# Kernel optimization log

Measured on AMD Instinct MI355X. Metric: run time of the kernel, lower is better.

## Reference

```python
import jax, jax.numpy as jnp
import numpy as np

B, T, E = 8, 2048, 1024
H = 16
HD = E // H            # per-head hidden_dim = 64
DFF = 4 * E
DC = T // 512          # decay_constant = 4
EPS = 1e-5


def setup_inputs() -> dict:
    key = jax.random.key(0)
    ks = jax.random.split(key, 8)
    return {
        "x": jax.random.normal(ks[0], (B, T, E), jnp.float32),
        # per-head input projections (Linear(dim, hidden_dim) x H)
        "w_proj": jax.random.normal(ks[1], (H, E, HD), jnp.float32) / np.sqrt(E),
        "b_proj": jnp.zeros((H, HD), jnp.float32),
        # causal mixing weights: first H//2 heads are Col-repeat, last H//2 Row-repeat
        "mix_w": jax.random.normal(ks[2], (H, T), jnp.float32),
        "mix_b": jnp.zeros((H, T), jnp.float32),
        "decay": jnp.ones((H,), jnp.float32),   # decay_value params (init ones as in torch)
        "out_w": jax.random.normal(ks[3], (E, E), jnp.float32) / np.sqrt(E),
        "out_b": jnp.zeros((E,), jnp.float32),
        "ln1_g": jnp.ones((E,), jnp.float32),
        "ln1_b": jnp.zeros((E,), jnp.float32),
        "ln2_g": jnp.ones((E,), jnp.float32),
        "ln2_b": jnp.zeros((E,), jnp.float32),
        "ff_w1": jax.random.normal(ks[4], (E, DFF), jnp.float32) / np.sqrt(E),
        "ff_b1": jnp.zeros((DFF,), jnp.float32),
        "ff_w2": jax.random.normal(ks[5], (DFF, E), jnp.float32) / np.sqrt(DFF),
        "ff_b2": jnp.zeros((E,), jnp.float32),
        "index": 0,
    }


def _layernorm(x, g, b):
    mu = jnp.mean(x, -1, keepdims=True)
    var = jnp.var(x, -1, keepdims=True)
    return (x - mu) * jax.lax.rsqrt(var + EPS) * g + b


def _mix_matrices(mix_w, decay):
    # Col heads: M[i,j] = v[j] * d**((j-i)/DC) for j>=i else 0
    # Row heads: M[i,j] = v[i] * d**((j-i)/DC) for j>=i else 0
    i = jnp.arange(T)[:, None]
    j = jnp.arange(T)[None, :]
    d = jnp.clip(decay, 0.9, 1.0)                                   # (H,)
    expo = (j - i).astype(jnp.float32) / DC                         # (T,T)
    dec = d[:, None, None] ** expo                                  # (H,T,T)
    causal = (j >= i)
    half = H // 2
    Mcol = jnp.where(causal, mix_w[:half, None, :] * dec[:half], 0.0)
    Mrow = jnp.where(causal, mix_w[half:, :, None] * dec[half:], 0.0)
    return jnp.concatenate([Mcol, Mrow], axis=0)                    # (H,T,T)


def reference(x, w_proj, b_proj, mix_w, mix_b, decay, out_w, out_b,
              ln1_g, ln1_b, ln2_g, ln2_b, ff_w1, ff_b1, ff_w2, ff_b2, index):
    # ---- token-mixing sub-block (parallel path of MixedRepeatHeads) ----
    res = x
    h = _layernorm(x, ln1_g, ln1_b)
    # per-head projection: (B,T,E) x (H,E,HD) -> (B,H,T,HD)
    p = jnp.einsum('bte,hef->bhtf', h, w_proj) + b_proj[:, None, :]
    M = _mix_matrices(mix_w, decay)
    # causal decay mixing along time: out[b,h,s,f] = sum_t p[b,h,t,f] * M[h,t,s]
    mixed = jnp.einsum('bhtf,hts->bhsf', p, M) + mix_b[None, :, :, None]
    # concat heads along feature dim -> (B,T,E)
    mixed = mixed.transpose(0, 2, 1, 3).reshape(B, T, E)
    mixed = mixed @ out_w + out_b
    x = mixed + res
    # ---- feed-forward sub-block ----
    res = x
    h = _layernorm(x, ln2_g, ln2_b)
    h = jax.nn.gelu(h @ ff_w1 + ff_b1) @ ff_w2 + ff_b2
    return h + res
```

## Files before the change

kernel.cpp:

```cpp
#include <hip/hip_runtime.h>


#define TT 2048
#define EE 1024
#define HHD 64
#define MROWS 16384
#define SC_L 64

typedef __bf16 bf16x8 __attribute__((ext_vector_type(8)));
typedef float f32x4 __attribute__((ext_vector_type(4)));
typedef unsigned short u16;
typedef unsigned int u32;

__device__ __forceinline__ u16 f2bf(float f) {
  u32 u = __builtin_bit_cast(u32, f);
  u += 0x7FFFu + ((u >> 16) & 1u);
  return (u16)(u >> 16);
}
__device__ __forceinline__ float bf2f(u16 s) {
  u32 u = ((u32)s) << 16;
  return __builtin_bit_cast(float, u);
}
__device__ __forceinline__ float gelu_f(float x) {
  float x2 = x * x;
  float e = -1.5957691216057308f * x * __builtin_fmaf(0.044715f, x2, 1.0f);
  return x * __builtin_amdgcn_rcpf(1.0f + __expf(e));
}
__device__ __forceinline__ void gload_lds16(const void* g, void* l) {
  __builtin_amdgcn_global_load_lds(
      (const __attribute__((address_space(1))) u32*)g,
      (__attribute__((address_space(3))) u32*)l, 16, 0, 0);
}
__device__ __forceinline__ void wg_barrier() {
  asm volatile("" ::: "memory");
  __builtin_amdgcn_s_barrier();
  asm volatile("" ::: "memory");
}

__global__ __launch_bounds__(256) void transpose_to_bf16(
    const float* __restrict__ src, u16* __restrict__ dst, int R, int C,
    long sbs, long dbs) {
  __shared__ float tile[32][33];
  src += (long)blockIdx.z * sbs;
  dst += (long)blockIdx.z * dbs;
  int c0 = blockIdx.x * 32, r0 = blockIdx.y * 32;
  int tx = threadIdx.x, ty = threadIdx.y;
#pragma unroll
  for (int i = 0; i < 4; i++)
    tile[ty + i * 8][tx] = src[(long)(r0 + ty + i * 8) * C + c0 + tx];
  __syncthreads();
#pragma unroll
  for (int i = 0; i < 4; i++)
    dst[(long)(c0 + ty + i * 8) * R + r0 + tx] = f2bf(tile[tx][ty + i * 8]);
}

__global__ __launch_bounds__(256) void ln_to_bf16(
    const float* __restrict__ x, const float* __restrict__ gam,
    const float* __restrict__ bet, u16* __restrict__ y) {
  int row = blockIdx.x;
  int tid = threadIdx.x;
  float4 v = ((const float4*)x)[row * 256 + tid];
  float s = v.x + v.y + v.z + v.w;
  float s2 = v.x * v.x + v.y * v.y + v.z * v.z + v.w * v.w;
#pragma unroll
  for (int off = 1; off < 64; off <<= 1) {
    s += __shfl_xor(s, off);
    s2 += __shfl_xor(s2, off);
  }
  __shared__ float red[8];
  int w = tid >> 6;
  if ((tid & 63) == 0) { red[w] = s; red[4 + w] = s2; }
  __syncthreads();
  s = red[0] + red[1] + red[2] + red[3];
  s2 = red[4] + red[5] + red[6] + red[7];
  float mu = s * (1.0f / 1024.0f);
  float var = s2 * (1.0f / 1024.0f) - mu * mu;
  float rstd = rsqrtf(var + 1e-5f);
  int e0 = tid * 4;
  ushort4 o;
  o.x = f2bf((v.x - mu) * rstd * gam[e0 + 0] + bet[e0 + 0]);
  o.y = f2bf((v.y - mu) * rstd * gam[e0 + 1] + bet[e0 + 1]);
  o.z = f2bf((v.z - mu) * rstd * gam[e0 + 2] + bet[e0 + 2]);
  o.w = f2bf((v.w - mu) * rstd * gam[e0 + 3] + bet[e0 + 3]);
  ((ushort4*)y)[row * 256 + tid] = o;
}

template <int EPI>
__global__ __launch_bounds__(512, 2) void gemm256(
    const u16* __restrict__ A, const u16* __restrict__ Bt,
    const float* __restrict__ bias, const float* __restrict__ res, void* outp,
    int M, int N, int K, int px, int gxp, int byper) {
  __shared__ u16 lds[65536];
  const int tid = threadIdx.x;
  const int w = tid >> 6, lane = tid & 63;
  const int wm = w >> 2, wn = w & 3;
  const int l15 = lane & 15, lk = lane >> 4;

  const int gx = (int)gridDim.x;
  const int bid = (int)blockIdx.y * gx + (int)blockIdx.x;
  const int xcd = bid & 7, i = bid >> 3;
  const int xg = xcd % gxp, yg = xcd / gxp;
  const int bx = xg * px + (i % px);
  const int by = yg * byper + (i / px);
  const int m0 = by * 256, n0 = bx * 256;

  const int srow = w * 8 + (lane >> 3);
  const int sslot = (lane & 7) ^ (lane >> 3);
  const u16* aS = A + (size_t)(m0 + srow) * K + sslot * 8;
  const u16* bS = Bt + (size_t)(n0 + srow) * K + sslot * 8;

  f32x4 acc[8][4];
  const f32x4 z = {0.f, 0.f, 0.f, 0.f};
#pragma unroll
  for (int mi = 0; mi < 8; mi++)
#pragma unroll
    for (int ni = 0; ni < 4; ni++) acc[mi][ni] = z;

  const int sl0 = (lk ^ (l15 & 7)) * 8;
  const int sl1 = ((4 + lk) ^ (l15 & 7)) * 8;

#define STAGE_ALL(C, KT) { \
    u16* lb = lds + (C) * 32768 + w * 512; \
    gload_lds16(bS + (KT), lb + 16384); \
    gload_lds16(bS + (size_t)64 * K + (KT), lb + 20480); \
    gload_lds16(bS + (size_t)128 * K + (KT), lb + 24576); \
    gload_lds16(bS + (size_t)192 * K + (KT), lb + 28672); \
    gload_lds16(aS + (KT), lb); \
    gload_lds16(aS + (size_t)64 * K + (KT), lb + 4096); \
    gload_lds16(aS + (size_t)128 * K + (KT), lb + 8192); \
    gload_lds16(aS + (size_t)192 * K + (KT), lb + 12288); }

  const int nt = K >> 6;
  STAGE_ALL(0, 0);

  for (int t = 0; t < nt; ++t) {
    const int cur = t & 1, nx = cur ^ 1;
    if (t + 1 < nt) {
      STAGE_ALL(nx, (t + 1) << 6);
      asm volatile("s_waitcnt vmcnt(8)" ::: "memory");
    } else {
      asm volatile("s_waitcnt vmcnt(0)" ::: "memory");
    }
    wg_barrier();

    const u16* lA = lds + cur * 32768;
    const u16* lB = lA + 16384;
    bf16x8 bq0[4], bq1[4];
    {
      const u16* bp = lB + (wn * 64 + l15) * 64;
#pragma unroll
      for (int ni = 0; ni < 4; ni++) {
        bq0[ni] = *(const bf16x8*)(bp + ni * 1024 + sl0);
        bq1[ni] = *(const bf16x8*)(bp + ni * 1024 + sl1);
      }
    }
#pragma unroll
    for (int mi = 0; mi < 8; mi++) {
      const u16* ap = lA + (wm * 128 + mi * 16 + l15) * 64;
      bf16x8 a0 = *(const bf16x8*)(ap + sl0);
      bf16x8 a1 = *(const bf16x8*)(ap + sl1);
      __builtin_amdgcn_s_setprio(1);
#pragma unroll
      for (int ni = 0; ni < 4; ni++)
        acc[mi][ni] = __builtin_amdgcn_mfma_f32_16x16x32_bf16(a0, bq0[ni],
                                                              acc[mi][ni], 0, 0, 0);
#pragma unroll
      for (int ni = 0; ni < 4; ni++)
        acc[mi][ni] = __builtin_amdgcn_mfma_f32_16x16x32_bf16(a1, bq1[ni],
                                                              acc[mi][ni], 0, 0, 0);
      __builtin_amdgcn_s_setprio(0);
    }
    wg_barrier();
  }
#undef STAGE_ALL

#pragma unroll
  for (int mi = 0; mi < 8; mi++) {
#pragma unroll
    for (int ni = 0; ni < 4; ni++) {
      int n = n0 + wn * 64 + ni * 16 + l15;
      float bvv = bias[n];
#pragma unroll
      for (int r = 0; r < 4; r++) {
        int m = m0 + wm * 128 + mi * 16 + lk * 4 + r;
        size_t idx = (size_t)m * N + n;
        float v = acc[mi][ni][r] + bvv;
        if (EPI == 0) {
          ((u16*)outp)[idx] = f2bf(v);
        } else if (EPI == 1) {
          ((float*)outp)[idx] = v + res[idx];
        } else {
          ((u16*)outp)[idx] = f2bf(gelu_f(v));
        }
      }
    }
  }
}

__global__ __launch_bounds__(64) void scan_carry(
    const u16* __restrict__ p, const float* __restrict__ mix_w,
    const float* __restrict__ decay, float* __restrict__ carry) {
  int blk = blockIdx.x;
  int c = blk & 31, h = (blk >> 5) & 15, b = blk >> 9;
  int f = threadIdx.x;
  float d = fminf(fmaxf(decay[h], 0.9f), 1.0f);
  float r = powf(d, 0.25f);
  size_t base = ((size_t)b * TT + c * SC_L) * EE + h * HHD + f;
  const float* mw = mix_w + h * TT + c * SC_L;
  bool isRow = (h >= 8);
  float S = 0.f;
#pragma unroll 4
  for (int t = 0; t < SC_L; t++) {
    float pv = bf2f(p[base + (size_t)t * EE]);
    float q = isRow ? mw[t] * pv : pv;
    S = r * S + q;
  }
  carry[blk * 64 + f] = S;
}

__global__ __launch_bounds__(64) void scan_apply(
    const u16* __restrict__ p, const float* __restrict__ mix_w,
    const float* __restrict__ mix_b, const float* __restrict__ decay,
    const float* __restrict__ carry, u16* __restrict__ mixed) {
  int blk = blockIdx.x;
  int c = blk & 31, h = (blk >> 5) & 15, b = blk >> 9;
  int f = threadIdx.x;
  float d = fminf(fmaxf(decay[h], 0.9f), 1.0f);
  float r = powf(d, 0.25f);
  float rl = powf(r, (float)SC_L);
  int cb = blk - c;
  float S = 0.f;
  for (int cc = 0; cc < c; cc++) S = rl * S + carry[(cb + cc) * 64 + f];
  size_t base = ((size_t)b * TT + c * SC_L) * EE + h * HHD + f;
  const float* mw = mix_w + h * TT + c * SC_L;
  const float* mb = mix_b + h * TT + c * SC_L;
  bool isRow = (h >= 8);
  for (int t = 0; t < SC_L; t++) {
    float pv = bf2f(p[base + (size_t)t * EE]);
    float q = isRow ? mw[t] * pv : pv;
    S = r * S + q;
    float val = (isRow ? S : mw[t] * S) + mb[t];
    mixed[base + (size_t)t * EE] = f2bf(val);
  }
}

extern "C" void kernel_launch(void* const* d_in, const int* in_sizes, int n_in,
                              void* d_out, int out_size, void* d_ws, size_t ws_size,
                              hipStream_t stream) {
  const float* x = (const float*)d_in[0];
  const float* w_proj = (const float*)d_in[1];
  const float* b_proj = (const float*)d_in[2];
  const float* mix_w = (const float*)d_in[3];
  const float* mix_b = (const float*)d_in[4];
  const float* decay = (const float*)d_in[5];
  const float* out_w = (const float*)d_in[6];
  const float* out_b = (const float*)d_in[7];
  const float* ln1_g = (const float*)d_in[8];
  const float* ln1_b = (const float*)d_in[9];
  const float* ln2_g = (const float*)d_in[10];
  const float* ln2_b = (const float*)d_in[11];
  const float* ff_w1 = (const float*)d_in[12];
  const float* ff_b1 = (const float*)d_in[13];
  const float* ff_w2 = (const float*)d_in[14];
  const float* ff_b2 = (const float*)d_in[15];
  float* out = (float*)d_out;

  char* ws = (char*)d_ws;
  const size_t MiB = 1ull << 20;
  u16* wWp = (u16*)(ws + 0 * MiB);
  u16* wWo = (u16*)(ws + 2 * MiB);
  u16* wW1 = (u16*)(ws + 4 * MiB);
  u16* wW2 = (u16*)(ws + 12 * MiB);
  u16* wMix = (u16*)(ws + 20 * MiB);
  u16* wH = (u16*)(ws + 52 * MiB);
  u16* wP = (u16*)(ws + 84 * MiB);
  u16* wU = (u16*)(ws + 52 * MiB);
  float* wCarry = (float*)(ws + 180 * MiB);

  dim3 tb(32, 8);
  transpose_to_bf16<<<dim3(2, 32, 16), tb, 0, stream>>>(w_proj, wWp, 1024, 64,
                                                        65536L, 65536L);
  transpose_to_bf16<<<dim3(32, 32, 1), tb, 0, stream>>>(out_w, wWo, 1024, 1024, 0L, 0L);
  transpose_to_bf16<<<dim3(128, 32, 1), tb, 0, stream>>>(ff_w1, wW1, 1024, 4096, 0L, 0L);
  transpose_to_bf16<<<dim3(32, 128, 1), tb, 0, stream>>>(ff_w2, wW2, 4096, 1024, 0L, 0L);

  ln_to_bf16<<<dim3(MROWS), dim3(256), 0, stream>>>(x, ln1_g, ln1_b, wH);

  gemm256<0><<<dim3(4, 64), dim3(512), 0, stream>>>(
      wH, wWp, b_proj, (const float*)nullptr, (void*)wP, MROWS, 1024, 1024,
      4, 1, 8);

  scan_carry<<<dim3(4096), dim3(64), 0, stream>>>(wP, mix_w, decay, wCarry);
  scan_apply<<<dim3(4096), dim3(64), 0, stream>>>(wP, mix_w, mix_b, decay, wCarry, wMix);

  gemm256<1><<<dim3(4, 64), dim3(512), 0, stream>>>(
      wMix, wWo, out_b, x, (void*)out, MROWS, 1024, 1024,
      4, 1, 8);

  ln_to_bf16<<<dim3(MROWS), dim3(256), 0, stream>>>(out, ln2_g, ln2_b, wMix);

  gemm256<2><<<dim3(16, 64), dim3(512), 0, stream>>>(
      wMix, wW1, ff_b1, (const float*)nullptr, (void*)wU, MROWS, 4096, 1024,
      4, 4, 32);

  gemm256<1><<<dim3(4, 64), dim3(512), 0, stream>>>(
      wU, wW2, ff_b2, out, (void*)out, MROWS, 1024, 4096,
      2, 2, 16);
}
```

Baseline: 551.2 us.

## Replace 256x256 GEMM tiles with 128x128 tiles and 32-wide K steps

Replaces the 512-thread 256x256-tile GEMM, which uses 64-wide K steps and 128 KB of LDS, with a 256-thread 128x128-tile kernel that uses 32-wide K steps, 32 KB of LDS and a new swizzle. Grid sizes and the XCD tile-mapping parameters change to match, giving four times as many blocks and higher occupancy per CU. The trade-off is lower arithmetic intensity per tile and more global loads and barriers per FLOP.

```diff
diff --git a/kernel.cpp b/kernel.cpp
--- a/kernel.cpp
+++ b/kernel.cpp
@@ -86,103 +86,89 @@
 }
 
 template <int EPI>
-__global__ __launch_bounds__(512, 2) void gemm256(
+__global__ __launch_bounds__(256, 4) void gemm128(
     const u16* __restrict__ A, const u16* __restrict__ Bt,
     const float* __restrict__ bias, const float* __restrict__ res, void* outp,
     int M, int N, int K, int px, int gxp, int byper) {
-  __shared__ u16 lds[65536];
+  __shared__ u16 lds[16384];
   const int tid = threadIdx.x;
   const int w = tid >> 6, lane = tid & 63;
-  const int wm = w >> 2, wn = w & 3;
+  const int wm = w >> 1, wn = w & 1;
   const int l15 = lane & 15, lk = lane >> 4;
 
   const int gx = (int)gridDim.x;
   const int bid = (int)blockIdx.y * gx + (int)blockIdx.x;
   const int xcd = bid & 7, i = bid >> 3;
-  const int xg = xcd % gxp, yg = xcd / gxp;
-  const int bx = xg * px + (i % px);
-  const int by = yg * byper + (i / px);
-  const int m0 = by * 256, n0 = bx * 256;
-
-  const int srow = w * 8 + (lane >> 3);
-  const int sslot = (lane & 7) ^ (lane >> 3);
+  const int bx = (xcd % gxp) * px + (i % px);
+  const int by = (xcd / gxp) * byper + (i / px);
+  const int m0 = by * 128, n0 = bx * 128;
+
+  const int srow = w * 16 + (lane >> 2);
+  const int sslot = (lane & 3) ^ ((lane >> 3) & 3);
   const u16* aS = A + (size_t)(m0 + srow) * K + sslot * 8;
   const u16* bS = Bt + (size_t)(n0 + srow) * K + sslot * 8;
 
-  f32x4 acc[8][4];
+  const int slotp = (lk ^ ((l15 >> 1) & 3)) * 8;
+  const int aOff = (wm * 64 + l15) * 32 + slotp;
+  const int bOff = 4096 + (wn * 64 + l15) * 32 + slotp;
+
+  f32x4 acc[4][4];
   const f32x4 z = {0.f, 0.f, 0.f, 0.f};
 #pragma unroll
-  for (int mi = 0; mi < 8; mi++)
+  for (int mi = 0; mi < 4; mi++)
 #pragma unroll
     for (int ni = 0; ni < 4; ni++) acc[mi][ni] = z;
 
-  const int sl0 = (lk ^ (l15 & 7)) * 8;
-  const int sl1 = ((4 + lk) ^ (l15 & 7)) * 8;
-
-#define STAGE_ALL(C, KT) { \
-    u16* lb = lds + (C) * 32768 + w * 512; \
-    gload_lds16(bS + (KT), lb + 16384); \
-    gload_lds16(bS + (size_t)64 * K + (KT), lb + 20480); \
-    gload_lds16(bS + (size_t)128 * K + (KT), lb + 24576); \
-    gload_lds16(bS + (size_t)192 * K + (KT), lb + 28672); \
+#define STAGE(C, KT) { \
+    u16* lb = lds + (C) * 8192 + w * 512; \
     gload_lds16(aS + (KT), lb); \
-    gload_lds16(aS + (size_t)64 * K + (KT), lb + 4096); \
-    gload_lds16(aS + (size_t)128 * K + (KT), lb + 8192); \
-    gload_lds16(aS + (size_t)192 * K + (KT), lb + 12288); }
-
-  const int nt = K >> 6;
-  STAGE_ALL(0, 0);
+    gload_lds16(aS + (size_t)64 * K + (KT), lb + 2048); \
+    gload_lds16(bS + (KT), lb + 4096); \
+    gload_lds16(bS + (size_t)64 * K + (KT), lb + 6144); }
+
+  const int nt = K >> 5;
+  STAGE(0, 0);
+  asm volatile("s_waitcnt vmcnt(0)" ::: "memory");
+  wg_barrier();
 
   for (int t = 0; t < nt; ++t) {
-    const int cur = t & 1, nx = cur ^ 1;
+    const int cur = t & 1;
     if (t + 1 < nt) {
-      STAGE_ALL(nx, (t + 1) << 6);
-      asm volatile("s_waitcnt vmcnt(8)" ::: "memory");
+      STAGE(cur ^ 1, (t + 1) << 5);
+      asm volatile("s_waitcnt vmcnt(4)" ::: "memory");
     } else {
       asm volatile("s_waitcnt vmcnt(0)" ::: "memory");
     }
     wg_barrier();
 
-    const u16* lA = lds + cur * 32768;
-    const u16* lB = lA + 16384;
-    bf16x8 bq0[4], bq1[4];
-    {
-      const u16* bp = lB + (wn * 64 + l15) * 64;
-#pragma unroll
-      for (int ni = 0; ni < 4; ni++) {
-        bq0[ni] = *(const bf16x8*)(bp + ni * 1024 + sl0);
-        bq1[ni] = *(const bf16x8*)(bp + ni * 1024 + sl1);
-      }
+    const u16* base = lds + cur * 8192;
+    bf16x8 bf[4];
+#pragma unroll
+    for (int ni = 0; ni < 4; ni++)
+      bf[ni] = *(const bf16x8*)(base + bOff + ni * 512);
+    __builtin_amdgcn_s_setprio(1);
+#pragma unroll
+    for (int mi = 0; mi < 4; mi++) {
+      bf16x8 af = *(const bf16x8*)(base + aOff + mi * 512);
+#pragma unroll
+      for (int ni = 0; ni < 4; ni++)
+        acc[mi][ni] = __builtin_amdgcn_mfma_f32_16x16x32_bf16(af, bf[ni],
+                                                              acc[mi][ni], 0, 0, 0);
     }
-#pragma unroll
-    for (int mi = 0; mi < 8; mi++) {
-      const u16* ap = lA + (wm * 128 + mi * 16 + l15) * 64;
-      bf16x8 a0 = *(const bf16x8*)(ap + sl0);
-      bf16x8 a1 = *(const bf16x8*)(ap + sl1);
-      __builtin_amdgcn_s_setprio(1);
-#pragma unroll
-      for (int ni = 0; ni < 4; ni++)
-        acc[mi][ni] = __builtin_amdgcn_mfma_f32_16x16x32_bf16(a0, bq0[ni],
-                                                              acc[mi][ni], 0, 0, 0);
-#pragma unroll
-      for (int ni = 0; ni < 4; ni++)
-        acc[mi][ni] = __builtin_amdgcn_mfma_f32_16x16x32_bf16(a1, bq1[ni],
-                                                              acc[mi][ni], 0, 0, 0);
-      __builtin_amdgcn_s_setprio(0);
-    }
+    __builtin_amdgcn_s_setprio(0);
     wg_barrier();
   }
-#undef STAGE_ALL
-
-#pragma unroll
-  for (int mi = 0; mi < 8; mi++) {
+#undef STAGE
+
+#pragma unroll
+  for (int mi = 0; mi < 4; mi++) {
 #pragma unroll
     for (int ni = 0; ni < 4; ni++) {
       int n = n0 + wn * 64 + ni * 16 + l15;
       float bvv = bias[n];
 #pragma unroll
       for (int r = 0; r < 4; r++) {
-        int m = m0 + wm * 128 + mi * 16 + lk * 4 + r;
+        int m = m0 + wm * 64 + mi * 16 + lk * 4 + r;
         size_t idx = (size_t)m * N + n;
         float v = acc[mi][ni][r] + bvv;
         if (EPI == 0) {
@@ -286,24 +272,24 @@
 
   ln_to_bf16<<<dim3(MROWS), dim3(256), 0, stream>>>(x, ln1_g, ln1_b, wH);
 
-  gemm256<0><<<dim3(4, 64), dim3(512), 0, stream>>>(
+  gemm128<0><<<dim3(8, 128), dim3(256), 0, stream>>>(
       wH, wWp, b_proj, (const float*)nullptr, (void*)wP, MROWS, 1024, 1024,
-      4, 1, 8);
+      8, 1, 16);
 
   scan_carry<<<dim3(4096), dim3(64), 0, stream>>>(wP, mix_w, decay, wCarry);
   scan_apply<<<dim3(4096), dim3(64), 0, stream>>>(wP, mix_w, mix_b, decay, wCarry, wMix);
 
-  gemm256<1><<<dim3(4, 64), dim3(512), 0, stream>>>(
+  gemm128<1><<<dim3(8, 128), dim3(256), 0, stream>>>(
       wMix, wWo, out_b, x, (void*)out, MROWS, 1024, 1024,
-      4, 1, 8);
+      8, 1, 16);
 
   ln_to_bf16<<<dim3(MROWS), dim3(256), 0, stream>>>(out, ln2_g, ln2_b, wMix);
 
-  gemm256<2><<<dim3(16, 64), dim3(512), 0, stream>>>(
+  gemm128<2><<<dim3(32, 128), dim3(256), 0, stream>>>(
       wMix, wW1, ff_b1, (const float*)nullptr, (void*)wU, MROWS, 4096, 1024,
-      4, 4, 32);
-
-  gemm256<1><<<dim3(4, 64), dim3(512), 0, stream>>>(
+      8, 4, 64);
+
+  gemm128<1><<<dim3(8, 128), dim3(256), 0, stream>>>(
       wU, wW2, ff_b2, out, (void*)out, MROWS, 1024, 4096,
-      2, 2, 16);
-}
+      2, 4, 64);
+}
```

Result: slower. 593.3 us (+7.6%).

## Add dedicated producer wave for GEMM global-to-LDS loads

Applied to the files above, without the earlier changes.

Reworks the GEMM into producer/consumer form. A ninth wave now issues every global-to-LDS tile load, and the eight compute waves only read LDS and run MFMAs, with barriers keeping the two in step. Launch bounds change from 512 threads with 2 blocks per CU to 576 threads with 1 block per CU. A single wave issuing 64 loads per stage, with a full vmcnt(0) wait each time, may become the bottleneck, and halving occupancy removes overlap between blocks.

```diff
diff --git a/kernel.cpp b/kernel.cpp
--- a/kernel.cpp
+++ b/kernel.cpp
@@ -86,28 +86,56 @@
 }
 
 template <int EPI>
-__global__ __launch_bounds__(512, 2) void gemm256(
+__global__ __launch_bounds__(576, 1) void gemm256pc(
     const u16* __restrict__ A, const u16* __restrict__ Bt,
     const float* __restrict__ bias, const float* __restrict__ res, void* outp,
     int M, int N, int K, int px, int gxp, int byper) {
   __shared__ u16 lds[65536];
   const int tid = threadIdx.x;
   const int w = tid >> 6, lane = tid & 63;
-  const int wm = w >> 2, wn = w & 3;
-  const int l15 = lane & 15, lk = lane >> 4;
 
   const int gx = (int)gridDim.x;
   const int bid = (int)blockIdx.y * gx + (int)blockIdx.x;
   const int xcd = bid & 7, i = bid >> 3;
-  const int xg = xcd % gxp, yg = xcd / gxp;
-  const int bx = xg * px + (i % px);
-  const int by = yg * byper + (i / px);
+  const int bx = (xcd % gxp) * px + (i % px);
+  const int by = (xcd / gxp) * byper + (i / px);
   const int m0 = by * 256, n0 = bx * 256;
 
-  const int srow = w * 8 + (lane >> 3);
-  const int sslot = (lane & 7) ^ (lane >> 3);
-  const u16* aS = A + (size_t)(m0 + srow) * K + sslot * 8;
-  const u16* bS = Bt + (size_t)(n0 + srow) * K + sslot * 8;
+  const int nt = K >> 6;
+
+  if (w == 8) {
+    const int rl = lane >> 3;
+    const int ssl = ((lane & 7) ^ (lane >> 3)) * 8;
+    const u16* aP = A + (size_t)(m0 + rl) * K + ssl;
+    const u16* bP = Bt + (size_t)(n0 + rl) * K + ssl;
+    const size_t cstride = (size_t)8 * K;
+
+#define PSTAGE(C, KT) { \
+    u16* lb = lds + (C) * 32768; \
+    _Pragma("unroll 8") \
+    for (int c = 0; c < 32; ++c) { \
+      gload_lds16(aP + (size_t)c * cstride + (KT), lb + c * 512); \
+      gload_lds16(bP + (size_t)c * cstride + (KT), lb + 16384 + c * 512); \
+    } }
+
+    PSTAGE(0, 0);
+    asm volatile("s_waitcnt vmcnt(0)" ::: "memory");
+    wg_barrier();
+    for (int t = 0; t < nt; ++t) {
+      if (t + 1 < nt) {
+        PSTAGE((t + 1) & 1, (t + 1) << 6);
+        asm volatile("s_waitcnt vmcnt(0)" ::: "memory");
+      }
+      wg_barrier();
+    }
+#undef PSTAGE
+    return;
+  }
+
+  const int wm = w >> 2, wn = w & 3;
+  const int l15 = lane & 15, lk = lane >> 4;
+  const int sl0 = (lk ^ (l15 & 7)) * 8;
+  const int sl1 = ((4 + lk) ^ (l15 & 7)) * 8;
 
   f32x4 acc[8][4];
   const f32x4 z = {0.f, 0.f, 0.f, 0.f};
@@ -116,33 +144,9 @@
 #pragma unroll
     for (int ni = 0; ni < 4; ni++) acc[mi][ni] = z;
 
-  const int sl0 = (lk ^ (l15 & 7)) * 8;
-  const int sl1 = ((4 + lk) ^ (l15 & 7)) * 8;
-
-#define STAGE_ALL(C, KT) { \
-    u16* lb = lds + (C) * 32768 + w * 512; \
-    gload_lds16(bS + (KT), lb + 16384); \
-    gload_lds16(bS + (size_t)64 * K + (KT), lb + 20480); \
-    gload_lds16(bS + (size_t)128 * K + (KT), lb + 24576); \
-    gload_lds16(bS + (size_t)192 * K + (KT), lb + 28672); \
-    gload_lds16(aS + (KT), lb); \
-    gload_lds16(aS + (size_t)64 * K + (KT), lb + 4096); \
-    gload_lds16(aS + (size_t)128 * K + (KT), lb + 8192); \
-    gload_lds16(aS + (size_t)192 * K + (KT), lb + 12288); }
-
-  const int nt = K >> 6;
-  STAGE_ALL(0, 0);
-
+  wg_barrier();
   for (int t = 0; t < nt; ++t) {
-    const int cur = t & 1, nx = cur ^ 1;
-    if (t + 1 < nt) {
-      STAGE_ALL(nx, (t + 1) << 6);
-      asm volatile("s_waitcnt vmcnt(8)" ::: "memory");
-    } else {
-      asm volatile("s_waitcnt vmcnt(0)" ::: "memory");
-    }
-    wg_barrier();
-
+    const int cur = t & 1;
     const u16* lA = lds + cur * 32768;
     const u16* lB = lA + 16384;
     bf16x8 bq0[4], bq1[4];
@@ -172,7 +176,6 @@
     }
     wg_barrier();
   }
-#undef STAGE_ALL
 
 #pragma unroll
   for (int mi = 0; mi < 8; mi++) {
@@ -286,24 +289,24 @@
 
   ln_to_bf16<<<dim3(MROWS), dim3(256), 0, stream>>>(x, ln1_g, ln1_b, wH);
 
-  gemm256<0><<<dim3(4, 64), dim3(512), 0, stream>>>(
+  gemm256pc<0><<<dim3(4, 64), dim3(576), 0, stream>>>(
       wH, wWp, b_proj, (const float*)nullptr, (void*)wP, MROWS, 1024, 1024,
       4, 1, 8);
 
   scan_carry<<<dim3(4096), dim3(64), 0, stream>>>(wP, mix_w, decay, wCarry);
   scan_apply<<<dim3(4096), dim3(64), 0, stream>>>(wP, mix_w, mix_b, decay, wCarry, wMix);
 
-  gemm256<1><<<dim3(4, 64), dim3(512), 0, stream>>>(
+  gemm256pc<1><<<dim3(4, 64), dim3(576), 0, stream>>>(
       wMix, wWo, out_b, x, (void*)out, MROWS, 1024, 1024,
       4, 1, 8);
 
   ln_to_bf16<<<dim3(MROWS), dim3(256), 0, stream>>>(out, ln2_g, ln2_b, wMix);
 
-  gemm256<2><<<dim3(16, 64), dim3(512), 0, stream>>>(
+  gemm256pc<2><<<dim3(16, 64), dim3(576), 0, stream>>>(
       wMix, wW1, ff_b1, (const float*)nullptr, (void*)wU, MROWS, 4096, 1024,
       4, 4, 32);
 
-  gemm256<1><<<dim3(4, 64), dim3(512), 0, stream>>>(
+  gemm256pc<1><<<dim3(4, 64), dim3(576), 0, stream>>>(
       wU, wW2, ff_b2, out, (void*)out, MROWS, 1024, 4096,
       2, 2, 16);
 }
```

Measured after the change: 698.3 us. 1.27x slower.

## Use 16-wave 1024-thread GEMM blocks with smaller per-wave accumulator tiles

Applied to the files above, without the earlier changes.

Each 256x256 GEMM tile is now computed by 16 waves instead of 8, each wave owning a 64x64 sub-tile (4x4 MFMA accumulators) rather than 128x64. Global-to-LDS staging is spread across twice as many threads, so each thread issues 4 loads per k-step instead of 8, and the wait count is adjusted to match. The aim is more waves per CU to hide latency and lower register pressure per wave. In exchange, each wave reuses B fragments across fewer A rows, so LDS reads per MFMA rise, and the old two-blocks-per-CU launch bound is dropped.

```diff
diff --git a/kernel.cpp b/kernel.cpp
--- a/kernel.cpp
+++ b/kernel.cpp
@@ -86,7 +86,7 @@
 }
 
 template <int EPI>
-__global__ __launch_bounds__(512, 2) void gemm256(
+__global__ __launch_bounds__(1024) void gemm256w16(
     const u16* __restrict__ A, const u16* __restrict__ Bt,
     const float* __restrict__ bias, const float* __restrict__ res, void* outp,
     int M, int N, int K, int px, int gxp, int byper) {
@@ -99,9 +99,8 @@
   const int gx = (int)gridDim.x;
   const int bid = (int)blockIdx.y * gx + (int)blockIdx.x;
   const int xcd = bid & 7, i = bid >> 3;
-  const int xg = xcd % gxp, yg = xcd / gxp;
-  const int bx = xg * px + (i % px);
-  const int by = yg * byper + (i / px);
+  const int bx = (xcd % gxp) * px + (i % px);
+  const int by = (xcd / gxp) * byper + (i / px);
   const int m0 = by * 256, n0 = bx * 256;
 
   const int srow = w * 8 + (lane >> 3);
@@ -109,10 +108,10 @@
   const u16* aS = A + (size_t)(m0 + srow) * K + sslot * 8;
   const u16* bS = Bt + (size_t)(n0 + srow) * K + sslot * 8;
 
-  f32x4 acc[8][4];
+  f32x4 acc[4][4];
   const f32x4 z = {0.f, 0.f, 0.f, 0.f};
 #pragma unroll
-  for (int mi = 0; mi < 8; mi++)
+  for (int mi = 0; mi < 4; mi++)
 #pragma unroll
     for (int ni = 0; ni < 4; ni++) acc[mi][ni] = z;
 
@@ -121,14 +120,10 @@
 
 #define STAGE_ALL(C, KT) { \
     u16* lb = lds + (C) * 32768 + w * 512; \
+    gload_lds16(aS + (KT), lb); \
+    gload_lds16(aS + (size_t)128 * K + (KT), lb + 8192); \
     gload_lds16(bS + (KT), lb + 16384); \
-    gload_lds16(bS + (size_t)64 * K + (KT), lb + 20480); \
-    gload_lds16(bS + (size_t)128 * K + (KT), lb + 24576); \
-    gload_lds16(bS + (size_t)192 * K + (KT), lb + 28672); \
-    gload_lds16(aS + (KT), lb); \
-    gload_lds16(aS + (size_t)64 * K + (KT), lb + 4096); \
-    gload_lds16(aS + (size_t)128 * K + (KT), lb + 8192); \
-    gload_lds16(aS + (size_t)192 * K + (KT), lb + 12288); }
+    gload_lds16(bS + (size_t)128 * K + (KT), lb + 24576); }
 
   const int nt = K >> 6;
   STAGE_ALL(0, 0);
@@ -137,37 +132,30 @@
     const int cur = t & 1, nx = cur ^ 1;
     if (t + 1 < nt) {
       STAGE_ALL(nx, (t + 1) << 6);
-      asm volatile("s_waitcnt vmcnt(8)" ::: "memory");
+      asm volatile("s_waitcnt vmcnt(4)" ::: "memory");
     } else {
       asm volatile("s_waitcnt vmcnt(0)" ::: "memory");
     }
     wg_barrier();
 
-    const u16* lA = lds + cur * 32768;
-    const u16* lB = lA + 16384;
-    bf16x8 bq0[4], bq1[4];
-    {
-      const u16* bp = lB + (wn * 64 + l15) * 64;
-#pragma unroll
-      for (int ni = 0; ni < 4; ni++) {
-        bq0[ni] = *(const bf16x8*)(bp + ni * 1024 + sl0);
-        bq1[ni] = *(const bf16x8*)(bp + ni * 1024 + sl1);
+    const u16* lA = lds + cur * 32768 + (wm * 64 + l15) * 64;
+    const u16* lB = lds + cur * 32768 + 16384 + (wn * 64 + l15) * 64;
+#pragma unroll
+    for (int ks = 0; ks < 2; ks++) {
+      const int sl = ks ? sl1 : sl0;
+      bf16x8 bq[4];
+#pragma unroll
+      for (int ni = 0; ni < 4; ni++)
+        bq[ni] = *(const bf16x8*)(lB + ni * 1024 + sl);
+      __builtin_amdgcn_s_setprio(1);
+#pragma unroll
+      for (int mi = 0; mi < 4; mi++) {
+        bf16x8 af = *(const bf16x8*)(lA + mi * 1024 + sl);
+#pragma unroll
+        for (int ni = 0; ni < 4; ni++)
+          acc[mi][ni] = __builtin_amdgcn_mfma_f32_16x16x32_bf16(af, bq[ni],
+                                                                acc[mi][ni], 0, 0, 0);
       }
-    }
-#pragma unroll
-    for (int mi = 0; mi < 8; mi++) {
-      const u16* ap = lA + (wm * 128 + mi * 16 + l15) * 64;
-      bf16x8 a0 = *(const bf16x8*)(ap + sl0);
-      bf16x8 a1 = *(const bf16x8*)(ap + sl1);
-      __builtin_amdgcn_s_setprio(1);
-#pragma unroll
-      for (int ni = 0; ni < 4; ni++)
-        acc[mi][ni] = __builtin_amdgcn_mfma_f32_16x16x32_bf16(a0, bq0[ni],
-                                                              acc[mi][ni], 0, 0, 0);
-#pragma unroll
-      for (int ni = 0; ni < 4; ni++)
-        acc[mi][ni] = __builtin_amdgcn_mfma_f32_16x16x32_bf16(a1, bq1[ni],
-                                                              acc[mi][ni], 0, 0, 0);
       __builtin_amdgcn_s_setprio(0);
     }
     wg_barrier();
@@ -175,14 +163,14 @@
 #undef STAGE_ALL
 
 #pragma unroll
-  for (int mi = 0; mi < 8; mi++) {
+  for (int mi = 0; mi < 4; mi++) {
 #pragma unroll
     for (int ni = 0; ni < 4; ni++) {
       int n = n0 + wn * 64 + ni * 16 + l15;
       float bvv = bias[n];
 #pragma unroll
       for (int r = 0; r < 4; r++) {
-        int m = m0 + wm * 128 + mi * 16 + lk * 4 + r;
+        int m = m0 + wm * 64 + mi * 16 + lk * 4 + r;
         size_t idx = (size_t)m * N + n;
         float v = acc[mi][ni][r] + bvv;
         if (EPI == 0) {
@@ -286,24 +274,24 @@
 
   ln_to_bf16<<<dim3(MROWS), dim3(256), 0, stream>>>(x, ln1_g, ln1_b, wH);
 
-  gemm256<0><<<dim3(4, 64), dim3(512), 0, stream>>>(
+  gemm256w16<0><<<dim3(4, 64), dim3(1024), 0, stream>>>(
       wH, wWp, b_proj, (const float*)nullptr, (void*)wP, MROWS, 1024, 1024,
       4, 1, 8);
 
   scan_carry<<<dim3(4096), dim3(64), 0, stream>>>(wP, mix_w, decay, wCarry);
   scan_apply<<<dim3(4096), dim3(64), 0, stream>>>(wP, mix_w, mix_b, decay, wCarry, wMix);
 
-  gemm256<1><<<dim3(4, 64), dim3(512), 0, stream>>>(
+  gemm256w16<1><<<dim3(4, 64), dim3(1024), 0, stream>>>(
       wMix, wWo, out_b, x, (void*)out, MROWS, 1024, 1024,
       4, 1, 8);
 
   ln_to_bf16<<<dim3(MROWS), dim3(256), 0, stream>>>(out, ln2_g, ln2_b, wMix);
 
-  gemm256<2><<<dim3(16, 64), dim3(512), 0, stream>>>(
+  gemm256w16<2><<<dim3(16, 64), dim3(1024), 0, stream>>>(
       wMix, wW1, ff_b1, (const float*)nullptr, (void*)wU, MROWS, 4096, 1024,
       4, 4, 32);
 
-  gemm256<1><<<dim3(4, 64), dim3(512), 0, stream>>>(
+  gemm256w16<1><<<dim3(4, 64), dim3(1024), 0, stream>>>(
       wU, wW2, ff_b2, out, (void*)out, MROWS, 1024, 4096,
       2, 2, 16);
 }
```

New measurement: 524.0 us. -4.9%, faster.
